# Optimization experiments

Hardware: AMD Instinct MI355X
Metric: run time of the kernel (lower is better)

Reference implementation:

```python
import jax, jax.numpy as jnp
import numpy as np

N = 50000      # nodes
E = 800000     # edges (avg degree 16)
FV = 128       # fv_dim (input node feature dim)
H = 128        # num_hiddens
EMB = 128      # node_embed_dim
OUT = 2        # out_ch


def _glorot(k, shape):
    lim = np.sqrt(6.0 / (shape[0] + shape[1]))
    return jax.random.uniform(k, shape, jnp.float32, -lim, lim)


def setup_inputs() -> dict:
    key = jax.random.key(0)
    ks = jax.random.split(key, 8)
    x = jax.random.normal(ks[0], (N, FV), jnp.float32)
    src = jax.random.randint(ks[1], (E,), 0, N, dtype=jnp.int32)
    dst = jax.random.randint(ks[2], (E,), 0, N, dtype=jnp.int32)
    W1 = _glorot(ks[3], (FV, H)); b1 = jnp.zeros((H,), jnp.float32)
    W2 = _glorot(ks[4], (H, H));  b2 = jnp.zeros((H,), jnp.float32)
    W3 = _glorot(ks[5], (H, EMB)); b3 = jnp.zeros((EMB,), jnp.float32)
    W_out = _glorot(ks[6], (EMB, OUT)); b_out = jnp.zeros((OUT,), jnp.float32)
    return dict(x=x, src=src, dst=dst, W1=W1, b1=b1, W2=W2, b2=b2,
                W3=W3, b3=b3, W_out=W_out, b_out=b_out)


def _gcn_layer(h, src, dst, norm_src, norm_dst, W, b):
    # DGL GraphConv, norm='both': h' = D_in^{-1/2} A D_out^{-1/2} h W + b
    h = h * norm_src                                  # scale by src out-degree
    m = jax.ops.segment_sum(h[src], dst, num_segments=N)  # gather + scatter-add
    m = m * norm_dst                                  # scale by dst in-degree
    return m @ W + b


def reference(x, src, dst, W1, b1, W2, b2, W3, b3, W_out, b_out):
    ones = jnp.ones((E,), x.dtype)
    deg_out = jax.ops.segment_sum(ones, src, num_segments=N)
    deg_in = jax.ops.segment_sum(ones, dst, num_segments=N)
    norm_src = jnp.maximum(deg_out, 1.0)[:, None] ** -0.5
    norm_dst = jnp.maximum(deg_in, 1.0)[:, None] ** -0.5

    h = jax.nn.elu(_gcn_layer(x, src, dst, norm_src, norm_dst, W1, b1))
    h = jax.nn.elu(_gcn_layer(h, src, dst, norm_src, norm_dst, W2, b2))
    n_embed = _gcn_layer(h, src, dst, norm_src, norm_dst, W3, b3)  # no activation
    n_out = n_embed @ W_out + b_out
    return (n_out, n_embed)
```

## Files before the change

kernel.cpp:

```cpp
#include <hip/hip_runtime.h>

#define N_NODES 50000
#define N_EDGES 800000
#define GRID_G 782
#define NB_HIST 128
#define EPB (N_EDGES / NB_HIST)
#define WORDS 25000
#define NORMB_BLOCKS 98

__global__ __launch_bounds__(256) void k_hist(const int* __restrict__ src,
                                              const int* __restrict__ dst,
                                              unsigned int* __restrict__ partO,
                                              unsigned int* __restrict__ partI) {
    __shared__ unsigned int h[12500];
    const int e0 = blockIdx.x * EPB;
    for (int kind = 0; kind < 2; ++kind) {
        const int* ids = kind ? dst : src;
        unsigned int* out = kind ? partI : partO;
        for (int p = 0; p < 2; ++p) {
            for (int i = threadIdx.x; i < 12500; i += 256) h[i] = 0;
            __syncthreads();
            const int base = p * 25000;
            for (int i = threadIdx.x; i < EPB; i += 256) {
                int id = ids[e0 + i] - base;
                if ((unsigned)id < 25000u)
                    atomicAdd(&h[id >> 1], (id & 1) ? 0x10000u : 1u);
            }
            __syncthreads();
            unsigned int* o = out + blockIdx.x * WORDS + p * 12500;
            for (int i = threadIdx.x; i < 12500; i += 256) o[i] = h[i];
            __syncthreads();
        }
    }
}

__global__ __launch_bounds__(256) void k_normB(const unsigned int* __restrict__ partO,
                                               const unsigned int* __restrict__ partI,
                                               float* __restrict__ norm_src,
                                               float* __restrict__ norm_dst,
                                               int* __restrict__ deg_in,
                                               int* __restrict__ partials98) {
    __shared__ int sm4[4];
    int w = blockIdx.x * 256 + threadIdx.x;
    unsigned int lo_o = 0, hi_o = 0, lo_i = 0, hi_i = 0;
    if (w < WORDS) {
        for (int b = 0; b < NB_HIST; ++b) {
            unsigned int vo = partO[b * WORDS + w];
            unsigned int vi = partI[b * WORDS + w];
            lo_o += vo & 0xFFFFu; hi_o += vo >> 16;
            lo_i += vi & 0xFFFFu; hi_i += vi >> 16;
        }
        int n0 = 2 * w;
        *(float2*)&norm_src[n0] = make_float2(rsqrtf((float)max(lo_o, 1u)),
                                              rsqrtf((float)max(hi_o, 1u)));
        *(float2*)&norm_dst[n0] = make_float2(rsqrtf((float)max(lo_i, 1u)),
                                              rsqrtf((float)max(hi_i, 1u)));
        *(int2*)&deg_in[n0] = make_int2((int)lo_i, (int)hi_i);
    }
    int v = (int)(lo_i + hi_i);
#pragma unroll
    for (int off = 32; off > 0; off >>= 1) v += __shfl_down(v, off);
    int lane = threadIdx.x & 63, wv = threadIdx.x >> 6;
    if (lane == 0) sm4[wv] = v;
    __syncthreads();
    if (threadIdx.x == 0)
        partials98[blockIdx.x] = sm4[0] + sm4[1] + sm4[2] + sm4[3];
}

__global__ __launch_bounds__(256) void k_scan(const int* __restrict__ deg_in,
                                              const int* __restrict__ partials98,
                                              int* __restrict__ row_start,
                                              int* __restrict__ cursor) {
    __shared__ int sm[256];
    __shared__ int carry_s;
    int t = threadIdx.x;
    if (t < 64) {
        int acc = 0;
        for (int i = t; i < blockIdx.x; i += 64) acc += partials98[i];
#pragma unroll
        for (int off = 32; off > 0; off >>= 1) acc += __shfl_down(acc, off);
        if (t == 0) carry_s = acc;
    }
    int n0 = blockIdx.x * 512 + t * 2;
    int a0 = 0, a1 = 0;
    if (n0 + 1 < N_NODES) {
        int2 d = *(const int2*)&deg_in[n0];
        a0 = d.x; a1 = d.y;
    } else if (n0 < N_NODES) {
        a0 = deg_in[n0];
    }
    sm[t] = a0 + a1;
    __syncthreads();
#pragma unroll
    for (int off = 1; off < 256; off <<= 1) {
        int tv = (t >= off) ? sm[t - off] : 0;
        __syncthreads();
        sm[t] += tv;
        __syncthreads();
    }
    int excl = sm[t] - (a0 + a1) + carry_s;
    if (n0 < N_NODES) { row_start[n0] = excl; cursor[n0] = excl; }
    if (n0 + 1 < N_NODES) { row_start[n0 + 1] = excl + a0; cursor[n0 + 1] = excl + a0; }
    if (blockIdx.x == 0 && t == 0) row_start[N_NODES] = N_EDGES;
}

__device__ __forceinline__ void gemm_body(const float* __restrict__ X,
                                          const float* __restrict__ W,
                                          float* __restrict__ G,
                                          float* __restrict__ Wl, int bid) {
    const int tx = threadIdx.x & 15;
    const int ty = threadIdx.x >> 4;
    const int r0 = bid * 64 + ty * 4;
    const int c0 = tx * 4;

    const float* xr[4];
#pragma unroll
    for (int i = 0; i < 4; ++i) {
        int r = r0 + i; if (r > N_NODES - 1) r = N_NODES - 1;
        xr[i] = X + (size_t)r * 128;
    }

    float acc[2][4][4] = {};
    for (int kc = 0; kc < 2; ++kc) {
        __syncthreads();
#pragma unroll
        for (int it = 0; it < 8; ++it) {
            int idx = threadIdx.x * 4 + it * 1024;
            *(float4*)&Wl[idx] = *(const float4*)&W[kc * 8192 + idx];
        }
        __syncthreads();
        const int kb = kc * 64;
        float4 xa[4], xb[4];
#pragma unroll
        for (int i = 0; i < 4; ++i) xa[i] = *(const float4*)(xr[i] + kb);
#pragma unroll 2
        for (int ks = 0; ks < 64; ks += 4) {
            const int kpf = (ks + 4 < 64) ? ks + 4 : ks;
#pragma unroll
            for (int i = 0; i < 4; ++i) xb[i] = *(const float4*)(xr[i] + kb + kpf);
#pragma unroll
            for (int kk = 0; kk < 4; ++kk) {
                float4 w0 = *(const float4*)&Wl[(ks + kk) * 128 + c0];
                float4 w1 = *(const float4*)&Wl[(ks + kk) * 128 + c0 + 64];
#pragma unroll
                for (int i = 0; i < 4; ++i) {
                    float a = (kk == 0) ? xa[i].x : (kk == 1) ? xa[i].y
                             : (kk == 2) ? xa[i].z : xa[i].w;
                    acc[0][i][0] = fmaf(a, w0.x, acc[0][i][0]);
                    acc[0][i][1] = fmaf(a, w0.y, acc[0][i][1]);
                    acc[0][i][2] = fmaf(a, w0.z, acc[0][i][2]);
                    acc[0][i][3] = fmaf(a, w0.w, acc[0][i][3]);
                    acc[1][i][0] = fmaf(a, w1.x, acc[1][i][0]);
                    acc[1][i][1] = fmaf(a, w1.y, acc[1][i][1]);
                    acc[1][i][2] = fmaf(a, w1.z, acc[1][i][2]);
                    acc[1][i][3] = fmaf(a, w1.w, acc[1][i][3]);
                }
            }
#pragma unroll
            for (int i = 0; i < 4; ++i) xa[i] = xb[i];
        }
    }
#pragma unroll
    for (int i = 0; i < 4; ++i) {
        int r = r0 + i;
        if (r < N_NODES) {
            float* p = G + (size_t)r * 128 + c0;
            *(float4*)p = make_float4(acc[0][i][0], acc[0][i][1], acc[0][i][2], acc[0][i][3]);
            *(float4*)(p + 64) = make_float4(acc[1][i][0], acc[1][i][1], acc[1][i][2], acc[1][i][3]);
        }
    }
}

__global__ __launch_bounds__(256, 4) void k_gemm(const float* __restrict__ X,
                                                 const float* __restrict__ W,
                                                 float* __restrict__ G) {
    __shared__ float Wl[8192];
    gemm_body(X, W, G, Wl, blockIdx.x);
}

__global__ __launch_bounds__(256, 4) void k_gemm_fill(const float* __restrict__ X,
                                                      const float* __restrict__ W,
                                                      float* __restrict__ G,
                                                      const int* __restrict__ src,
                                                      const int* __restrict__ dst,
                                                      const float* __restrict__ norm_src,
                                                      int* __restrict__ cursor,
                                                      int2* __restrict__ csr) {
    __shared__ float Wl[8192];
    if (blockIdx.x < GRID_G) {
        gemm_body(X, W, G, Wl, blockIdx.x);
    } else {
        int e = (blockIdx.x - GRID_G) * 256 + threadIdx.x;
        if (e < N_EDGES) {
            int d = dst[e], s = src[e];
            int pos = atomicAdd(&cursor[d], 1);
            csr[pos] = make_int2(s, __float_as_int(norm_src[s]));
        }
    }
}

template <int ELU, int PROJ>
__global__ __launch_bounds__(256) void k_gather(const float* __restrict__ G,
                                                const int* __restrict__ row_start,
                                                const int2* __restrict__ csr,
                                                const float* __restrict__ norm_dst,
                                                const float* __restrict__ bias,
                                                float* __restrict__ Out,
                                                const float* __restrict__ Wo,
                                                const float* __restrict__ bo,
                                                float* __restrict__ proj_out) {
    int n = (blockIdx.x * 256 + threadIdx.x) >> 6;
    int lane = threadIdx.x & 63;
    if (n >= N_NODES) return;
    const int half = lane >> 5;
    const int l = lane & 31;
    int e0 = row_start[n], e1 = row_start[n + 1];
    float4 a0 = {0,0,0,0}, a1 = {0,0,0,0}, a2 = {0,0,0,0}, a3 = {0,0,0,0};
    int e = e0;
    for (; e + 8 <= e1; e += 8) {
        int2 c0 = csr[e + half],     c1 = csr[e + 2 + half];
        int2 c2 = csr[e + 4 + half], c3 = csr[e + 6 + half];
        float4 g0 = *(const float4*)(G + (size_t)c0.x * 128 + l * 4);
        float4 g1 = *(const float4*)(G + (size_t)c1.x * 128 + l * 4);
        float4 g2 = *(const float4*)(G + (size_t)c2.x * 128 + l * 4);
        float4 g3 = *(const float4*)(G + (size_t)c3.x * 128 + l * 4);
        float w0 = __int_as_float(c0.y), w1 = __int_as_float(c1.y);
        float w2 = __int_as_float(c2.y), w3 = __int_as_float(c3.y);
        a0.x = fmaf(w0, g0.x, a0.x); a0.y = fmaf(w0, g0.y, a0.y);
        a0.z = fmaf(w0, g0.z, a0.z); a0.w = fmaf(w0, g0.w, a0.w);
        a1.x = fmaf(w1, g1.x, a1.x); a1.y = fmaf(w1, g1.y, a1.y);
        a1.z = fmaf(w1, g1.z, a1.z); a1.w = fmaf(w1, g1.w, a1.w);
        a2.x = fmaf(w2, g2.x, a2.x); a2.y = fmaf(w2, g2.y, a2.y);
        a2.z = fmaf(w2, g2.z, a2.z); a2.w = fmaf(w2, g2.w, a2.w);
        a3.x = fmaf(w3, g3.x, a3.x); a3.y = fmaf(w3, g3.y, a3.y);
        a3.z = fmaf(w3, g3.z, a3.z); a3.w = fmaf(w3, g3.w, a3.w);
    }
    for (; e < e1; e += 2) {
        int idx = e + half;
        if (idx < e1) {
            int2 c = csr[idx];
            float w = __int_as_float(c.y);
            float4 g = *(const float4*)(G + (size_t)c.x * 128 + l * 4);
            a0.x = fmaf(w, g.x, a0.x); a0.y = fmaf(w, g.y, a0.y);
            a0.z = fmaf(w, g.z, a0.z); a0.w = fmaf(w, g.w, a0.w);
        }
    }
    float4 s;
    s.x = (a0.x + a1.x) + (a2.x + a3.x);
    s.y = (a0.y + a1.y) + (a2.y + a3.y);
    s.z = (a0.z + a1.z) + (a2.z + a3.z);
    s.w = (a0.w + a1.w) + (a2.w + a3.w);
    s.x += __shfl_xor(s.x, 32);
    s.y += __shfl_xor(s.y, 32);
    s.z += __shfl_xor(s.z, 32);
    s.w += __shfl_xor(s.w, 32);
    float nd = norm_dst[n];
    float4 b = *(const float4*)(bias + l * 4);
    float4 o;
    o.x = fmaf(nd, s.x, b.x);
    o.y = fmaf(nd, s.y, b.y);
    o.z = fmaf(nd, s.z, b.z);
    o.w = fmaf(nd, s.w, b.w);
    if (ELU) {
        o.x = o.x > 0.f ? o.x : expm1f(o.x);
        o.y = o.y > 0.f ? o.y : expm1f(o.y);
        o.z = o.z > 0.f ? o.z : expm1f(o.z);
        o.w = o.w > 0.f ? o.w : expm1f(o.w);
    }
    if (half == 0)
        *(float4*)(Out + (size_t)n * 128 + l * 4) = o;
    if (PROJ) {
        float p0 = o.x * Wo[(l * 4 + 0) * 2] + o.y * Wo[(l * 4 + 1) * 2]
                 + o.z * Wo[(l * 4 + 2) * 2] + o.w * Wo[(l * 4 + 3) * 2];
        float p1 = o.x * Wo[(l * 4 + 0) * 2 + 1] + o.y * Wo[(l * 4 + 1) * 2 + 1]
                 + o.z * Wo[(l * 4 + 2) * 2 + 1] + o.w * Wo[(l * 4 + 3) * 2 + 1];
#pragma unroll
        for (int off = 16; off > 0; off >>= 1) {
            p0 += __shfl_down(p0, off);
            p1 += __shfl_down(p1, off);
        }
        if (lane == 0) {
            proj_out[n * 2 + 0] = p0 + bo[0];
            proj_out[n * 2 + 1] = p1 + bo[1];
        }
    }
}

extern "C" void kernel_launch(void* const* d_in, const int* in_sizes, int n_in,
                              void* d_out, int out_size, void* d_ws, size_t ws_size,
                              hipStream_t stream) {
    const float* x     = (const float*)d_in[0];
    const int*   src   = (const int*)d_in[1];
    const int*   dst   = (const int*)d_in[2];
    const float* W1    = (const float*)d_in[3];
    const float* b1    = (const float*)d_in[4];
    const float* W2    = (const float*)d_in[5];
    const float* b2    = (const float*)d_in[6];
    const float* W3    = (const float*)d_in[7];
    const float* b3    = (const float*)d_in[8];
    const float* W_out = (const float*)d_in[9];
    const float* b_out = (const float*)d_in[10];

    float* out = (float*)d_out;
    float* emb = out + (size_t)N_NODES * 2;

    char* ws = (char*)d_ws;
    float* norm_src  = (float*)(ws + 0);
    float* norm_dst  = (float*)(ws + 200192);
    int*   deg_in    = (int*)(ws + 400384);
    int*   row_start = (int*)(ws + 600576);
    int*   cursor    = (int*)(ws + 801280);
    int*   partials98= (int*)(ws + 1001472);
    int2*  csr       = (int2*)(ws + 1001984);
    float* bufA      = (float*)(ws + 7401984);
    float* bufB      = (float*)(ws + 33001984);
    unsigned int* partO = (unsigned int*)bufA;
    unsigned int* partI = partO + (size_t)NB_HIST * WORDS;

    const int gridW = (N_NODES * 64 + 255) / 256;
    const int gridF = GRID_G + (N_EDGES + 255) / 256;

    k_hist<<<NB_HIST, 256, 0, stream>>>(src, dst, partO, partI);
    k_normB<<<NORMB_BLOCKS, 256, 0, stream>>>(partO, partI, norm_src, norm_dst,
                                              deg_in, partials98);
    k_scan<<<NORMB_BLOCKS, 256, 0, stream>>>(deg_in, partials98, row_start, cursor);
    k_gemm_fill<<<gridF, 256, 0, stream>>>(x, W1, bufB, src, dst, norm_src,
                                           cursor, csr);
    k_gather<1, 0><<<gridW, 256, 0, stream>>>(bufB, row_start, csr, norm_dst, b1,
                                              bufA, nullptr, nullptr, nullptr);
    k_gemm<<<GRID_G, 256, 0, stream>>>(bufA, W2, bufB);
    k_gather<1, 0><<<gridW, 256, 0, stream>>>(bufB, row_start, csr, norm_dst, b2,
                                              bufA, nullptr, nullptr, nullptr);
    k_gemm<<<GRID_G, 256, 0, stream>>>(bufA, W3, bufB);
    k_gather<0, 1><<<gridW, 256, 0, stream>>>(bufB, row_start, csr, norm_dst, b3,
                                              emb, W_out, b_out, out);
}
```

Baseline: 329.2 us.

## Fuse gather-aggregate with following GEMM for layers two and three

Layers 2 and 3 now aggregate first and transform after (A·H then W), with the aggregation result kept in an LDS tile and multiplied by W inside the same kernel. This removes the separate GEMM launches and one full 50000x128 intermediate write and read per layer. The output projection is folded algebraically into a precomputed W3·W_out and bias, applied to the tile. In exchange, each block now does the gather with only 4 waves over 16 nodes each, which lowers the memory-level parallelism of the gather, and it uses more LDS per block.

```diff
diff --git a/kernel.cpp b/kernel.cpp
--- a/kernel.cpp
+++ b/kernel.cpp
@@ -7,6 +7,26 @@
 #define EPB (N_EDGES / NB_HIST)
 #define WORDS 25000
 #define NORMB_BLOCKS 98
+#define TILE_LD 132
+
+__global__ __launch_bounds__(256) void k_wfuse(const float* __restrict__ W3,
+                                               const float* __restrict__ Wout,
+                                               const float* __restrict__ b3,
+                                               const float* __restrict__ bout,
+                                               float* __restrict__ Wf,
+                                               float* __restrict__ bf) {
+    int t = threadIdx.x;
+    int j = t >> 1, c = t & 1;
+    float acc = 0.f;
+    for (int k = 0; k < 128; ++k)
+        acc += W3[j * 128 + k] * Wout[k * 2 + c];
+    Wf[j * 2 + c] = acc;
+    if (t < 2) {
+        float a = bout[t];
+        for (int k = 0; k < 128; ++k) a += b3[k] * Wout[k * 2 + t];
+        bf[t] = a;
+    }
+}
 
 __global__ __launch_bounds__(256) void k_hist(const int* __restrict__ src,
                                               const int* __restrict__ dst,
@@ -171,13 +191,6 @@
     }
 }
 
-__global__ __launch_bounds__(256, 4) void k_gemm(const float* __restrict__ X,
-                                                 const float* __restrict__ W,
-                                                 float* __restrict__ G) {
-    __shared__ float Wl[8192];
-    gemm_body(X, W, G, Wl, blockIdx.x);
-}
-
 __global__ __launch_bounds__(256, 4) void k_gemm_fill(const float* __restrict__ X,
                                                       const float* __restrict__ W,
                                                       float* __restrict__ G,
@@ -199,16 +212,12 @@
     }
 }
 
-template <int ELU, int PROJ>
 __global__ __launch_bounds__(256) void k_gather(const float* __restrict__ G,
                                                 const int* __restrict__ row_start,
                                                 const int2* __restrict__ csr,
                                                 const float* __restrict__ norm_dst,
                                                 const float* __restrict__ bias,
-                                                float* __restrict__ Out,
-                                                const float* __restrict__ Wo,
-                                                const float* __restrict__ bo,
-                                                float* __restrict__ proj_out) {
+                                                float* __restrict__ Out) {
     int n = (blockIdx.x * 256 + threadIdx.x) >> 6;
     int lane = threadIdx.x & 63;
     if (n >= N_NODES) return;
@@ -261,27 +270,165 @@
     o.y = fmaf(nd, s.y, b.y);
     o.z = fmaf(nd, s.z, b.z);
     o.w = fmaf(nd, s.w, b.w);
-    if (ELU) {
-        o.x = o.x > 0.f ? o.x : expm1f(o.x);
-        o.y = o.y > 0.f ? o.y : expm1f(o.y);
-        o.z = o.z > 0.f ? o.z : expm1f(o.z);
-        o.w = o.w > 0.f ? o.w : expm1f(o.w);
-    }
+    o.x = o.x > 0.f ? o.x : expm1f(o.x);
+    o.y = o.y > 0.f ? o.y : expm1f(o.y);
+    o.z = o.z > 0.f ? o.z : expm1f(o.z);
+    o.w = o.w > 0.f ? o.w : expm1f(o.w);
     if (half == 0)
         *(float4*)(Out + (size_t)n * 128 + l * 4) = o;
+}
+
+template <int ELU, int PROJ>
+__global__ __launch_bounds__(256, 4) void k_fused(const float* __restrict__ Hin,
+                                                  const int* __restrict__ row_start,
+                                                  const int2* __restrict__ csr,
+                                                  const float* __restrict__ norm_dst,
+                                                  const float* __restrict__ W,
+                                                  const float* __restrict__ bias,
+                                                  float* __restrict__ Out,
+                                                  const float* __restrict__ Wf,
+                                                  const float* __restrict__ bf,
+                                                  float* __restrict__ proj_out) {
+    __shared__ float tile[64 * TILE_LD];
+    __shared__ float Wl[4096];
+    const int tid = threadIdx.x;
+    const int bid = blockIdx.x;
+    const int lane = tid & 63;
+    const int wv = tid >> 6;
+    const int half = lane >> 5;
+    const int l = lane & 31;
+
+    for (int i = 0; i < 16; ++i) {
+        const int nl = wv * 16 + i;
+        const int n = bid * 64 + nl;
+        if (n >= N_NODES) break;
+        int e0 = row_start[n], e1 = row_start[n + 1];
+        float4 a0 = {0,0,0,0}, a1 = {0,0,0,0}, a2 = {0,0,0,0}, a3 = {0,0,0,0};
+        int e = e0;
+        for (; e + 8 <= e1; e += 8) {
+            int2 c0 = csr[e + half],     c1 = csr[e + 2 + half];
+            int2 c2 = csr[e + 4 + half], c3 = csr[e + 6 + half];
+            float4 g0 = *(const float4*)(Hin + (size_t)c0.x * 128 + l * 4);
+            float4 g1 = *(const float4*)(Hin + (size_t)c1.x * 128 + l * 4);
+            float4 g2 = *(const float4*)(Hin + (size_t)c2.x * 128 + l * 4);
+            float4 g3 = *(const float4*)(Hin + (size_t)c3.x * 128 + l * 4);
+            float w0 = __int_as_float(c0.y), w1 = __int_as_float(c1.y);
+            float w2 = __int_as_float(c2.y), w3 = __int_as_float(c3.y);
+            a0.x = fmaf(w0, g0.x, a0.x); a0.y = fmaf(w0, g0.y, a0.y);
+            a0.z = fmaf(w0, g0.z, a0.z); a0.w = fmaf(w0, g0.w, a0.w);
+            a1.x = fmaf(w1, g1.x, a1.x); a1.y = fmaf(w1, g1.y, a1.y);
+            a1.z = fmaf(w1, g1.z, a1.z); a1.w = fmaf(w1, g1.w, a1.w);
+            a2.x = fmaf(w2, g2.x, a2.x); a2.y = fmaf(w2, g2.y, a2.y);
+            a2.z = fmaf(w2, g2.z, a2.z); a2.w = fmaf(w2, g2.w, a2.w);
+            a3.x = fmaf(w3, g3.x, a3.x); a3.y = fmaf(w3, g3.y, a3.y);
+            a3.z = fmaf(w3, g3.z, a3.z); a3.w = fmaf(w3, g3.w, a3.w);
+        }
+        for (; e < e1; e += 2) {
+            int idx = e + half;
+            if (idx < e1) {
+                int2 c = csr[idx];
+                float w = __int_as_float(c.y);
+                float4 g = *(const float4*)(Hin + (size_t)c.x * 128 + l * 4);
+                a0.x = fmaf(w, g.x, a0.x); a0.y = fmaf(w, g.y, a0.y);
+                a0.z = fmaf(w, g.z, a0.z); a0.w = fmaf(w, g.w, a0.w);
+            }
+        }
+        float4 s;
+        s.x = (a0.x + a1.x) + (a2.x + a3.x);
+        s.y = (a0.y + a1.y) + (a2.y + a3.y);
+        s.z = (a0.z + a1.z) + (a2.z + a3.z);
+        s.w = (a0.w + a1.w) + (a2.w + a3.w);
+        s.x += __shfl_xor(s.x, 32);
+        s.y += __shfl_xor(s.y, 32);
+        s.z += __shfl_xor(s.z, 32);
+        s.w += __shfl_xor(s.w, 32);
+        float nd = norm_dst[n];
+        if (half == 0) {
+            *(float4*)&tile[nl * TILE_LD + l * 4] =
+                make_float4(nd * s.x, nd * s.y, nd * s.z, nd * s.w);
+        }
+    }
+    __syncthreads();
+
+    const int tx = tid & 15;
+    const int ty = tid >> 4;
+    const int c0 = tx * 4;
+    float acc[2][4][4] = {};
+    for (int kc = 0; kc < 4; ++kc) {
+        __syncthreads();
+#pragma unroll
+        for (int it = 0; it < 4; ++it) {
+            int idx = tid * 4 + it * 1024;
+            *(float4*)&Wl[idx] = *(const float4*)&W[kc * 4096 + idx];
+        }
+        __syncthreads();
+        const int kb = kc * 32;
+#pragma unroll 2
+        for (int ks = 0; ks < 32; ks += 4) {
+            float4 xa[4];
+#pragma unroll
+            for (int i = 0; i < 4; ++i)
+                xa[i] = *(const float4*)&tile[(ty * 4 + i) * TILE_LD + kb + ks];
+#pragma unroll
+            for (int kk = 0; kk < 4; ++kk) {
+                float4 w0 = *(const float4*)&Wl[(ks + kk) * 128 + c0];
+                float4 w1 = *(const float4*)&Wl[(ks + kk) * 128 + c0 + 64];
+#pragma unroll
+                for (int i = 0; i < 4; ++i) {
+                    float a = (kk == 0) ? xa[i].x : (kk == 1) ? xa[i].y
+                             : (kk == 2) ? xa[i].z : xa[i].w;
+                    acc[0][i][0] = fmaf(a, w0.x, acc[0][i][0]);
+                    acc[0][i][1] = fmaf(a, w0.y, acc[0][i][1]);
+                    acc[0][i][2] = fmaf(a, w0.z, acc[0][i][2]);
+                    acc[0][i][3] = fmaf(a, w0.w, acc[0][i][3]);
+                    acc[1][i][0] = fmaf(a, w1.x, acc[1][i][0]);
+                    acc[1][i][1] = fmaf(a, w1.y, acc[1][i][1]);
+                    acc[1][i][2] = fmaf(a, w1.z, acc[1][i][2]);
+                    acc[1][i][3] = fmaf(a, w1.w, acc[1][i][3]);
+                }
+            }
+        }
+    }
+    float4 bb0 = *(const float4*)&bias[c0];
+    float4 bb1 = *(const float4*)&bias[c0 + 64];
+#pragma unroll
+    for (int i = 0; i < 4; ++i) {
+        int r = bid * 64 + ty * 4 + i;
+        if (r < N_NODES) {
+            float4 o0 = make_float4(acc[0][i][0] + bb0.x, acc[0][i][1] + bb0.y,
+                                    acc[0][i][2] + bb0.z, acc[0][i][3] + bb0.w);
+            float4 o1 = make_float4(acc[1][i][0] + bb1.x, acc[1][i][1] + bb1.y,
+                                    acc[1][i][2] + bb1.z, acc[1][i][3] + bb1.w);
+            if (ELU) {
+                o0.x = o0.x > 0.f ? o0.x : expm1f(o0.x);
+                o0.y = o0.y > 0.f ? o0.y : expm1f(o0.y);
+                o0.z = o0.z > 0.f ? o0.z : expm1f(o0.z);
+                o0.w = o0.w > 0.f ? o0.w : expm1f(o0.w);
+                o1.x = o1.x > 0.f ? o1.x : expm1f(o1.x);
+                o1.y = o1.y > 0.f ? o1.y : expm1f(o1.y);
+                o1.z = o1.z > 0.f ? o1.z : expm1f(o1.z);
+                o1.w = o1.w > 0.f ? o1.w : expm1f(o1.w);
+            }
+            float* p = Out + (size_t)r * 128 + c0;
+            *(float4*)p = o0;
+            *(float4*)(p + 64) = o1;
+        }
+    }
+
     if (PROJ) {
-        float p0 = o.x * Wo[(l * 4 + 0) * 2] + o.y * Wo[(l * 4 + 1) * 2]
-                 + o.z * Wo[(l * 4 + 2) * 2] + o.w * Wo[(l * 4 + 3) * 2];
-        float p1 = o.x * Wo[(l * 4 + 0) * 2 + 1] + o.y * Wo[(l * 4 + 1) * 2 + 1]
-                 + o.z * Wo[(l * 4 + 2) * 2 + 1] + o.w * Wo[(l * 4 + 3) * 2 + 1];
-#pragma unroll
-        for (int off = 16; off > 0; off >>= 1) {
-            p0 += __shfl_down(p0, off);
-            p1 += __shfl_down(p1, off);
-        }
-        if (lane == 0) {
-            proj_out[n * 2 + 0] = p0 + bo[0];
-            proj_out[n * 2 + 1] = p1 + bo[1];
+        if (tid < 128) {
+            int nl = tid >> 1, c = tid & 1;
+            int n = bid * 64 + nl;
+            if (n < N_NODES) {
+                float accp = bf[c];
+#pragma unroll 8
+                for (int k = 0; k < 128; k += 4) {
+                    float4 g = *(const float4*)&tile[nl * TILE_LD + k];
+                    accp += g.x * Wf[(k + 0) * 2 + c] + g.y * Wf[(k + 1) * 2 + c]
+                          + g.z * Wf[(k + 2) * 2 + c] + g.w * Wf[(k + 3) * 2 + c];
+                }
+                proj_out[n * 2 + c] = accp;
+            }
         }
     }
 }
@@ -311,27 +458,27 @@
     int*   row_start = (int*)(ws + 600576);
     int*   cursor    = (int*)(ws + 801280);
     int*   partials98= (int*)(ws + 1001472);
-    int2*  csr       = (int2*)(ws + 1001984);
-    float* bufA      = (float*)(ws + 7401984);
-    float* bufB      = (float*)(ws + 33001984);
+    float* Wf        = (float*)(ws + 1001984);
+    float* bf        = (float*)(ws + 1003008);
+    int2*  csr       = (int2*)(ws + 1003520);
+    float* bufA      = (float*)(ws + 7403520);
+    float* bufB      = (float*)(ws + 33003520);
     unsigned int* partO = (unsigned int*)bufA;
     unsigned int* partI = partO + (size_t)NB_HIST * WORDS;
 
     const int gridW = (N_NODES * 64 + 255) / 256;
     const int gridF = GRID_G + (N_EDGES + 255) / 256;
 
+    k_wfuse<<<1, 256, 0, stream>>>(W3, W_out, b3, b_out, Wf, bf);
     k_hist<<<NB_HIST, 256, 0, stream>>>(src, dst, partO, partI);
     k_normB<<<NORMB_BLOCKS, 256, 0, stream>>>(partO, partI, norm_src, norm_dst,
                                               deg_in, partials98);
     k_scan<<<NORMB_BLOCKS, 256, 0, stream>>>(deg_in, partials98, row_start, cursor);
     k_gemm_fill<<<gridF, 256, 0, stream>>>(x, W1, bufB, src, dst, norm_src,
                                            cursor, csr);
-    k_gather<1, 0><<<gridW, 256, 0, stream>>>(bufB, row_start, csr, norm_dst, b1,
-                                              bufA, nullptr, nullptr, nullptr);
-    k_gemm<<<GRID_G, 256, 0, stream>>>(bufA, W2, bufB);
-    k_gather<1, 0><<<gridW, 256, 0, stream>>>(bufB, row_start, csr, norm_dst, b2,
-                                              bufA, nullptr, nullptr, nullptr);
-    k_gemm<<<GRID_G, 256, 0, stream>>>(bufA, W3, bufB);
-    k_gather<0, 1><<<gridW, 256, 0, stream>>>(bufB, row_start, csr, norm_dst, b3,
-                                              emb, W_out, b_out, out);
-}
+    k_gather<<<gridW, 256, 0, stream>>>(bufB, row_start, csr, norm_dst, b1, bufA);
+    k_fused<1, 0><<<GRID_G, 256, 0, stream>>>(bufA, row_start, csr, norm_dst,
+                                              W2, b2, bufB, nullptr, nullptr, nullptr);
+    k_fused<0, 1><<<GRID_G, 256, 0, stream>>>(bufB, row_start, csr, norm_dst,
+                                              W3, b3, emb, Wf, bf, out);
+}
```

Measured after the change: 413.8 us. +25.7%, slower.
